# Kernel tuning notes

Measured on AMD Instinct MI355X. Metric: run time of the kernel, lower is better.

Reference implementation:

```python
import jax, jax.numpy as jnp
import numpy as np

V, E, B, C = 10000, 128, 16, 128
N_REL = 8

def setup_inputs() -> dict:
    key = jax.random.key(0)
    k1, k2, k3, k4, k5 = jax.random.split(key, 5)
    src = jax.random.randint(k1, (B, C), 0, V, dtype=jnp.int32)
    src_embed = jax.random.normal(k2, (B, C, E), dtype=jnp.float32)
    embed_weight = jax.random.normal(k3, (V, E), dtype=jnp.float32)
    edge_matrix = jax.random.uniform(k4, (V, V), dtype=jnp.float32)
    relation_matrix = jax.random.randint(k5, (V, V), 0, 9, dtype=jnp.int32)
    return {"src": src, "src_embed": src_embed, "embed_weight": embed_weight,
            "edge_matrix": edge_matrix, "relation_matrix": relation_matrix}

def reference(src, src_embed, embed_weight, edge_matrix, relation_matrix):
    # base scores against full vocab: [B, C, V]
    base = jnp.einsum('bce,ve->bcv', src_embed, embed_weight)
    # gather the rows of both tables once: [B, C, V]
    edge_rows = edge_matrix[src]
    rel_rows = relation_matrix[src]
    concept_embeddings = []
    scores = []
    for i in range(N_REL):
        # ((relation_matrix == i+1) * edge_matrix)[src] > 0, gathered form
        mask = (jnp.where(rel_rows == i + 1, edge_rows, 0.0) > 0).astype(base.dtype)
        concept_weights = mask * base                     # [B, C, V]
        attn = jax.nn.softmax(concept_weights, axis=2)     # softmax over full vocab
        ce = jnp.einsum('bcv,ve->bce', attn, embed_weight) # [B, C, E]
        concept_embeddings.append(ce)
        scores.append(jnp.sum(src_embed * ce, axis=2, keepdims=True))
    scores = jnp.concatenate(scores, axis=2)               # [B, C, 8]
    weights = jax.nn.softmax(scores, axis=2)
    final = jnp.zeros_like(src_embed)
    for i in range(N_REL):
        final = final + weights[:, :, i:i + 1] * concept_embeddings[i]
    return final
```

## Files before the change

kernel.cpp:

```cpp
#include <hip/hip_runtime.h>

#define VV 10000
#define EE 128
#define NROWS 2048
#define KS 32
#define RBSTRIDE 5120

typedef unsigned short u16;
using short8 = __attribute__((ext_vector_type(8))) short;
using f32x4  = __attribute__((ext_vector_type(4))) float;

__device__ __forceinline__ u16 f2bf(float x) {
    unsigned u = __float_as_uint(x);
    return (u16)((u + 0x7fffu + ((u >> 16) & 1u)) >> 16);
}
__device__ __forceinline__ float bf2f(u16 h) {
    return __uint_as_float(((unsigned)h) << 16);
}

__global__ __launch_bounds__(256) void k0_prep(
    const float* __restrict__ SE,
    const float* __restrict__ W,
    u16* __restrict__ SEh, u16* __restrict__ SEl,
    u16* __restrict__ Wh,  u16* __restrict__ Wl,
    u16* __restrict__ WTh, u16* __restrict__ WTl)
{
    const int u = blockIdx.x * 256 + threadIdx.x;
    float x[8];
    u16 *dh, *dl;

    if (u < 32768) {
        int fid = u >> 6, l = u & 63;
        int nf = fid >> 2, kt = fid & 3;
        int row = nf * 16 + (l & 15);
        int k0 = kt * 32 + (l >> 4) * 8;
        const float* p = SE + row * EE + k0;
        float4 a = *(const float4*)p, b = *(const float4*)(p + 4);
        x[0]=a.x; x[1]=a.y; x[2]=a.z; x[3]=a.w;
        x[4]=b.x; x[5]=b.y; x[6]=b.z; x[7]=b.w;
        dh = SEh + u * 8; dl = SEl + u * 8;
    } else if (u < 192768) {
        int u2 = u - 32768;
        int fid = u2 >> 6, l = u2 & 63;
        int vf = fid >> 2, kt = fid & 3;
        int row = vf * 16 + (l & 15);
        int k0 = kt * 32 + (l >> 4) * 8;
        const float* p = W + row * EE + k0;
        float4 a = *(const float4*)p, b = *(const float4*)(p + 4);
        x[0]=a.x; x[1]=a.y; x[2]=a.z; x[3]=a.w;
        x[4]=b.x; x[5]=b.y; x[6]=b.z; x[7]=b.w;
        dh = Wh + u2 * 8; dl = Wl + u2 * 8;
    } else {
        int u3 = u - 192768;
        int fid = u3 >> 6, l = u3 & 63;
        int ef = fid / 313, kc = fid - ef * 313;
        int e  = ef * 16 + (l & 15);
        int k8 = kc * 32 + (l >> 4) * 8;
        if (k8 < VV) {
            #pragma unroll
            for (int i = 0; i < 8; i++) x[i] = W[(k8 + i) * EE + e];
        } else {
            #pragma unroll
            for (int i = 0; i < 8; i++) x[i] = 0.f;
        }
        dh = WTh + u3 * 8; dl = WTl + u3 * 8;
    }

    short8 hv, lv;
    #pragma unroll
    for (int i = 0; i < 8; i++) {
        u16 hb = f2bf(x[i]);
        hv[i] = (short)hb;
        lv[i] = (short)f2bf(x[i] - bf2f(hb));
    }
    *(short8*)dh = hv;
    *(short8*)dl = lv;
}

__global__ __launch_bounds__(256) void k1_mfma(
    const u16* __restrict__ SEh, const u16* __restrict__ SEl,
    const u16* __restrict__ Wh,  const u16* __restrict__ Wl,
    float* __restrict__ base)
{
    const int tid = threadIdx.x;
    const int l = tid & 63, wv = tid >> 6;
    const int wn = wv >> 1, wq = wv & 1;
    const int vt = blockIdx.y, nt = blockIdx.x;
    const int nf0 = nt * 4 + wn * 2;
    const int vf0 = vt * 8 + wq * 4;

    f32x4 acc[2][4];
    #pragma unroll
    for (int i = 0; i < 2; i++)
        #pragma unroll
        for (int j = 0; j < 4; j++)
            acc[i][j] = (f32x4){0.f, 0.f, 0.f, 0.f};

    #pragma unroll
    for (int kt = 0; kt < 4; ++kt) {
        short8 ah[2], al[2];
        #pragma unroll
        for (int i = 0; i < 2; ++i) {
            int off = (((nf0 + i) * 4 + kt) * 64 + l) * 8;
            ah[i] = *(const short8*)(SEh + off);
            al[i] = *(const short8*)(SEl + off);
        }
        #pragma unroll
        for (int j = 0; j < 4; ++j) {
            int vf = vf0 + j;
            short8 bh = {0,0,0,0,0,0,0,0};
            short8 bl = {0,0,0,0,0,0,0,0};
            if (vf < 625) {
                int off = ((vf * 4 + kt) * 64 + l) * 8;
                bh = *(const short8*)(Wh + off);
                bl = *(const short8*)(Wl + off);
            }
            #pragma unroll
            for (int i = 0; i < 2; ++i) {
                acc[i][j] = __builtin_amdgcn_mfma_f32_16x16x32_bf16(ah[i], bh, acc[i][j], 0, 0, 0);
                acc[i][j] = __builtin_amdgcn_mfma_f32_16x16x32_bf16(ah[i], bl, acc[i][j], 0, 0, 0);
                acc[i][j] = __builtin_amdgcn_mfma_f32_16x16x32_bf16(al[i], bh, acc[i][j], 0, 0, 0);
            }
        }
    }

    const int c = l & 15, r0 = (l >> 4) * 4;
    #pragma unroll
    for (int j = 0; j < 4; ++j) {
        int vf = vf0 + j;
        if (vf >= 625) continue;
        int v = vf * 16 + c;
        #pragma unroll
        for (int i = 0; i < 2; ++i) {
            int n = (nf0 + i) * 16 + r0;
            #pragma unroll
            for (int r = 0; r < 4; ++r)
                base[(n + r) * VV + v] = acc[i][j][r];
        }
    }
}

__global__ __launch_bounds__(256) void k2_stats(
    const int*   __restrict__ src,
    const float* __restrict__ edge,
    const int*   __restrict__ rel,
    const float* __restrict__ baseA,
    unsigned char* __restrict__ rb4,
    float* __restrict__ cG)
{
    __shared__ float wred[33][4];
    __shared__ float fin[33];

    const int n = blockIdx.x;
    const int tid = threadIdx.x;
    const int lane = tid & 63;
    const int wv = tid >> 6;
    const int s = src[n];
    const float4* brow4 = (const float4*)(baseA + (long long)n * VV);
    const float4* erow4 = (const float4*)(edge + (long long)s * VV);
    const int4*   rrow4 = (const int4*)(rel + (long long)s * VV);
    unsigned short* crow = (unsigned short*)(rb4 + (long long)n * RBSTRIDE);

    float accv[33];
    #pragma unroll
    for (int i = 0; i < 33; i++) accv[i] = 0.f;

    for (int v4 = tid; v4 < VV / 4; v4 += 256) {
        float4 b = brow4[v4];
        float4 e = erow4[v4];
        int4   r = rrow4[v4];
        float bb[4] = {b.x, b.y, b.z, b.w};
        float ee[4] = {e.x, e.y, e.z, e.w};
        int   rr[4] = {r.x, r.y, r.z, r.w};
        unsigned pk = 0u;
        #pragma unroll
        for (int c = 0; c < 4; c++) {
            int rb = (rr[c] >= 1 && rr[c] <= 8 && ee[c] > 0.f) ? rr[c] : 0;
            float bc = bb[c];
            float eb = __expf(bc);
            float beb = bc * eb;
            pk |= ((unsigned)rb) << (4 * c);
            accv[0] += bc;
            #pragma unroll
            for (int q = 0; q < 8; q++) {
                float m = (rb == q + 1) ? 1.f : 0.f;
                accv[1 + q]  += m;
                accv[9 + q]  = fmaf(m, bc,  accv[9 + q]);
                accv[17 + q] = fmaf(m, eb,  accv[17 + q]);
                accv[25 + q] = fmaf(m, beb, accv[25 + q]);
            }
        }
        crow[v4] = (unsigned short)pk;
    }

    #pragma unroll
    for (int i = 0; i < 33; i++) {
        float x = accv[i];
        #pragma unroll
        for (int off = 32; off > 0; off >>= 1) x += __shfl_xor(x, off, 64);
        if (lane == 0) wred[i][wv] = x;
    }
    __syncthreads();
    if (tid < 33)
        fin[tid] = wred[tid][0] + wred[tid][1] + wred[tid][2] + wred[tid][3];
    __syncthreads();

    if (tid == 0) {
        float sumbase = fin[0];
        float sc[8], Z[8];
        float smax = -1e30f;
        #pragma unroll
        for (int q = 0; q < 8; q++) {
            Z[q]  = ((float)VV - fin[1 + q]) + fin[17 + q];
            sc[q] = (sumbase - fin[9 + q] + fin[25 + q]) / Z[q];
            smax = fmaxf(smax, sc[q]);
        }
        float wsum = 0.f, wq[8];
        #pragma unroll
        for (int q = 0; q < 8; q++) { wq[q] = __expf(sc[q] - smax); wsum += wq[q]; }
        float Kc = 0.f;
        float* cg = cG + n * 10;
        #pragma unroll
        for (int q = 0; q < 8; q++) {
            float c = (wq[q] / wsum) / Z[q];
            cg[1 + q] = c;
            Kc += c;
        }
        cg[0] = 0.f;
        cg[9] = Kc;
    }
}

__global__ __launch_bounds__(256) void k3_mfma(
    const float* __restrict__ baseA,
    const unsigned char* __restrict__ rb4,
    const float* __restrict__ cG,
    const u16* __restrict__ WTh, const u16* __restrict__ WTl,
    float* __restrict__ part)
{
    __shared__ float cvt[64][10];

    const int tid = threadIdx.x;
    const int l = tid & 63, wv = tid >> 6;
    const int wm = wv >> 1, we = wv & 1;
    const int mt = blockIdx.x, ks = blockIdx.y;
    const int g = l >> 4, rr_ = l & 15;
    const int kc0 = (313 * ks) / KS;
    const int kc1 = (313 * (ks + 1)) / KS;

    for (int t = tid; t < 640; t += 256)
        cvt[t / 10][t % 10] = cG[(mt * 64 + t / 10) * 10 + (t % 10)];
    __syncthreads();

    const int mf0 = mt * 4 + wm * 2;
    const int rl0 = (wm * 2) * 16 + rr_;
    const int rl1 = (wm * 2 + 1) * 16 + rr_;
    const float* arow0 = baseA + (long long)(mf0 * 16 + rr_) * VV;
    const float* arow1 = baseA + (long long)((mf0 + 1) * 16 + rr_) * VV;
    const unsigned char* rrow0 = rb4 + (long long)(mf0 * 16 + rr_) * RBSTRIDE;
    const unsigned char* rrow1 = rb4 + (long long)((mf0 + 1) * 16 + rr_) * RBSTRIDE;
    const float Kc0 = cvt[rl0][9];
    const float Kc1 = cvt[rl1][9];

    f32x4 acc[2][4];
    #pragma unroll
    for (int i = 0; i < 2; i++)
        #pragma unroll
        for (int j = 0; j < 4; j++)
            acc[i][j] = (f32x4){0.f, 0.f, 0.f, 0.f};

    for (int kc = kc0; kc < kc1; ++kc) {
        int k8 = kc * 32 + g * 8;
        short8 ah[2], al[2];

        #pragma unroll
        for (int i = 0; i < 2; ++i) {
            const float* arow = i ? arow1 : arow0;
            const unsigned char* rrow = i ? rrow1 : rrow0;
            const float Kci = i ? Kc1 : Kc0;
            const int rli = i ? rl1 : rl0;
            float x[8];
            if (k8 < VV) {
                float4 a = *(const float4*)(arow + k8);
                float4 b = *(const float4*)(arow + k8 + 4);
                unsigned cw = *(const unsigned*)(rrow + (k8 >> 1));
                float t[8] = {a.x, a.y, a.z, a.w, b.x, b.y, b.z, b.w};
                #pragma unroll
                for (int q = 0; q < 8; q++) {
                    float cc = cvt[rli][(cw >> (4 * q)) & 15u];
                    x[q] = fmaf(cc, __expf(t[q]) - 1.f, Kci);
                }
            } else {
                #pragma unroll
                for (int q = 0; q < 8; q++) x[q] = 0.f;
            }
            #pragma unroll
            for (int q = 0; q < 8; q++) {
                u16 hb = f2bf(x[q]);
                ah[i][q] = (short)hb;
                al[i][q] = (short)f2bf(x[q] - bf2f(hb));
            }
        }

        #pragma unroll
        for (int j = 0; j < 4; ++j) {
            int ef = we * 4 + j;
            int off = ((ef * 313 + kc) * 64 + l) * 8;
            short8 bh = *(const short8*)(WTh + off);
            short8 bl = *(const short8*)(WTl + off);
            #pragma unroll
            for (int i = 0; i < 2; ++i) {
                acc[i][j] = __builtin_amdgcn_mfma_f32_16x16x32_bf16(ah[i], bh, acc[i][j], 0, 0, 0);
                acc[i][j] = __builtin_amdgcn_mfma_f32_16x16x32_bf16(ah[i], bl, acc[i][j], 0, 0, 0);
                acc[i][j] = __builtin_amdgcn_mfma_f32_16x16x32_bf16(al[i], bh, acc[i][j], 0, 0, 0);
            }
        }
    }

    float* pp = part + (long long)ks * NROWS * EE;
    const int c = l & 15, r0 = g * 4;
    #pragma unroll
    for (int i = 0; i < 2; ++i) {
        #pragma unroll
        for (int j = 0; j < 4; ++j) {
            int e = (we * 4 + j) * 16 + c;
            int m = (mf0 + i) * 16 + r0;
            #pragma unroll
            for (int r = 0; r < 4; ++r)
                pp[(m + r) * EE + e] = acc[i][j][r];
        }
    }
}

__global__ __launch_bounds__(256) void k4_reduce(
    const float* __restrict__ part, float* __restrict__ out)
{
    int idx = blockIdx.x * 256 + threadIdx.x;
    const float4* p = (const float4*)part;
    const int stride = NROWS * EE / 4;
    float4 s = p[idx];
    #pragma unroll
    for (int k = 1; k < KS; k++) {
        float4 t = p[idx + k * stride];
        s.x += t.x; s.y += t.y; s.z += t.z; s.w += t.w;
    }
    ((float4*)out)[idx] = s;
}

extern "C" void kernel_launch(void* const* d_in, const int* in_sizes, int n_in,
                              void* d_out, int out_size, void* d_ws, size_t ws_size,
                              hipStream_t stream) {
    const int*   src  = (const int*)  d_in[0];
    const float* SE   = (const float*)d_in[1];
    const float* W    = (const float*)d_in[2];
    const float* edge = (const float*)d_in[3];
    const int*   rel  = (const int*)  d_in[4];
    float* out  = (float*)d_out;

    float* base = (float*)d_ws;
    float* part = base + (long long)NROWS * VV;
    u16* SEh = (u16*)(part + (long long)KS * NROWS * EE);
    u16* SEl = SEh + 262144;
    u16* Wh  = SEl + 262144;
    u16* Wl  = Wh  + 1280000;
    u16* WTh = Wl  + 1280000;
    u16* WTl = WTh + 1282048;
    unsigned char* rb4 = (unsigned char*)(WTl + 1282048);
    float* cG = (float*)(rb4 + (long long)NROWS * RBSTRIDE);

    k0_prep<<<dim3(1379), 256, 0, stream>>>(SE, W, SEh, SEl, Wh, Wl, WTh, WTl);
    k1_mfma<<<dim3(32, 79), 256, 0, stream>>>(SEh, SEl, Wh, Wl, base);
    k2_stats<<<dim3(NROWS), 256, 0, stream>>>(src, edge, rel, base, rb4, cG);
    k3_mfma<<<dim3(32, KS), 256, 0, stream>>>(base, rb4, cG, WTh, WTl, part);
    k4_reduce<<<dim3(256), 256, 0, stream>>>(part, out);
}
```

Measured before the change: 715.1 us.

## Replace split-K partial buffer and reduce kernel with atomic accumulation in k3

```diff
diff --git a/kernel.cpp b/kernel.cpp
--- a/kernel.cpp
+++ b/kernel.cpp
@@ -16,6 +16,12 @@
 }
 __device__ __forceinline__ float bf2f(u16 h) {
     return __uint_as_float(((unsigned)h) << 16);
+}
+
+__global__ __launch_bounds__(256) void kz_zero(float* __restrict__ out)
+{
+    int idx = blockIdx.x * 256 + threadIdx.x;
+    ((float4*)out)[idx] = make_float4(0.f, 0.f, 0.f, 0.f);
 }
 
 __global__ __launch_bounds__(256) void k0_prep(
@@ -236,14 +242,15 @@
     const unsigned char* __restrict__ rb4,
     const float* __restrict__ cG,
     const u16* __restrict__ WTh, const u16* __restrict__ WTl,
-    float* __restrict__ part)
+    float* __restrict__ out)
 {
     __shared__ float cvt[64][10];
 
     const int tid = threadIdx.x;
     const int l = tid & 63, wv = tid >> 6;
-    const int wm = wv >> 1, we = wv & 1;
-    const int mt = blockIdx.x, ks = blockIdx.y;
+    const int fid = blockIdx.x;
+    const int ks = (fid & 7) * 4 + (fid >> 8);
+    const int mt = (fid >> 3) & 31;
     const int g = l >> 4, rr_ = l & 15;
     const int kc0 = (313 * ks) / KS;
     const int kc1 = (313 * (ks + 1)) / KS;
@@ -252,33 +259,21 @@
         cvt[t / 10][t % 10] = cG[(mt * 64 + t / 10) * 10 + (t % 10)];
     __syncthreads();
 
-    const int mf0 = mt * 4 + wm * 2;
-    const int rl0 = (wm * 2) * 16 + rr_;
-    const int rl1 = (wm * 2 + 1) * 16 + rr_;
-    const float* arow0 = baseA + (long long)(mf0 * 16 + rr_) * VV;
-    const float* arow1 = baseA + (long long)((mf0 + 1) * 16 + rr_) * VV;
-    const unsigned char* rrow0 = rb4 + (long long)(mf0 * 16 + rr_) * RBSTRIDE;
-    const unsigned char* rrow1 = rb4 + (long long)((mf0 + 1) * 16 + rr_) * RBSTRIDE;
-    const float Kc0 = cvt[rl0][9];
-    const float Kc1 = cvt[rl1][9];
-
-    f32x4 acc[2][4];
-    #pragma unroll
-    for (int i = 0; i < 2; i++)
-        #pragma unroll
-        for (int j = 0; j < 4; j++)
-            acc[i][j] = (f32x4){0.f, 0.f, 0.f, 0.f};
+    const int mf = mt * 4 + wv;
+    const int row = mf * 16 + rr_;
+    const int rl = wv * 16 + rr_;
+    const float* arow = baseA + (long long)row * VV;
+    const unsigned char* rrow = rb4 + (long long)row * RBSTRIDE;
+    const float Kc = cvt[rl][9];
+
+    f32x4 acc[8];
+    #pragma unroll
+    for (int j = 0; j < 8; j++) acc[j] = (f32x4){0.f, 0.f, 0.f, 0.f};
 
     for (int kc = kc0; kc < kc1; ++kc) {
         int k8 = kc * 32 + g * 8;
-        short8 ah[2], al[2];
-
-        #pragma unroll
-        for (int i = 0; i < 2; ++i) {
-            const float* arow = i ? arow1 : arow0;
-            const unsigned char* rrow = i ? rrow1 : rrow0;
-            const float Kci = i ? Kc1 : Kc0;
-            const int rli = i ? rl1 : rl0;
+        short8 ah, al;
+        {
             float x[8];
             if (k8 < VV) {
                 float4 a = *(const float4*)(arow + k8);
@@ -287,8 +282,8 @@
                 float t[8] = {a.x, a.y, a.z, a.w, b.x, b.y, b.z, b.w};
                 #pragma unroll
                 for (int q = 0; q < 8; q++) {
-                    float cc = cvt[rli][(cw >> (4 * q)) & 15u];
-                    x[q] = fmaf(cc, __expf(t[q]) - 1.f, Kci);
+                    float cc = cvt[rl][(cw >> (4 * q)) & 15u];
+                    x[q] = fmaf(cc, __expf(t[q]) - 1.f, Kc);
                 }
             } else {
                 #pragma unroll
@@ -297,54 +292,31 @@
             #pragma unroll
             for (int q = 0; q < 8; q++) {
                 u16 hb = f2bf(x[q]);
-                ah[i][q] = (short)hb;
-                al[i][q] = (short)f2bf(x[q] - bf2f(hb));
-            }
-        }
-
-        #pragma unroll
-        for (int j = 0; j < 4; ++j) {
-            int ef = we * 4 + j;
-            int off = ((ef * 313 + kc) * 64 + l) * 8;
+                ah[q] = (short)hb;
+                al[q] = (short)f2bf(x[q] - bf2f(hb));
+            }
+        }
+
+        #pragma unroll
+        for (int j = 0; j < 8; ++j) {
+            int off = ((j * 313 + kc) * 64 + l) * 8;
             short8 bh = *(const short8*)(WTh + off);
             short8 bl = *(const short8*)(WTl + off);
-            #pragma unroll
-            for (int i = 0; i < 2; ++i) {
-                acc[i][j] = __builtin_amdgcn_mfma_f32_16x16x32_bf16(ah[i], bh, acc[i][j], 0, 0, 0);
-                acc[i][j] = __builtin_amdgcn_mfma_f32_16x16x32_bf16(ah[i], bl, acc[i][j], 0, 0, 0);
-                acc[i][j] = __builtin_amdgcn_mfma_f32_16x16x32_bf16(al[i], bh, acc[i][j], 0, 0, 0);
-            }
-        }
-    }
-
-    float* pp = part + (long long)ks * NROWS * EE;
+            acc[j] = __builtin_amdgcn_mfma_f32_16x16x32_bf16(ah, bh, acc[j], 0, 0, 0);
+            acc[j] = __builtin_amdgcn_mfma_f32_16x16x32_bf16(ah, bl, acc[j], 0, 0, 0);
+            acc[j] = __builtin_amdgcn_mfma_f32_16x16x32_bf16(al, bh, acc[j], 0, 0, 0);
+        }
+    }
+
     const int c = l & 15, r0 = g * 4;
     #pragma unroll
-    for (int i = 0; i < 2; ++i) {
-        #pragma unroll
-        for (int j = 0; j < 4; ++j) {
-            int e = (we * 4 + j) * 16 + c;
-            int m = (mf0 + i) * 16 + r0;
-            #pragma unroll
-            for (int r = 0; r < 4; ++r)
-                pp[(m + r) * EE + e] = acc[i][j][r];
-        }
-    }
-}
-
-__global__ __launch_bounds__(256) void k4_reduce(
-    const float* __restrict__ part, float* __restrict__ out)
-{
-    int idx = blockIdx.x * 256 + threadIdx.x;
-    const float4* p = (const float4*)part;
-    const int stride = NROWS * EE / 4;
-    float4 s = p[idx];
-    #pragma unroll
-    for (int k = 1; k < KS; k++) {
-        float4 t = p[idx + k * stride];
-        s.x += t.x; s.y += t.y; s.z += t.z; s.w += t.w;
-    }
-    ((float4*)out)[idx] = s;
+    for (int j = 0; j < 8; ++j) {
+        int e = j * 16 + c;
+        int m = mf * 16 + r0;
+        #pragma unroll
+        for (int r = 0; r < 4; ++r)
+            atomicAdd(&out[(m + r) * EE + e], acc[j][r]);
+    }
 }
 
 extern "C" void kernel_launch(void* const* d_in, const int* in_sizes, int n_in,
@@ -358,8 +330,7 @@
     float* out  = (float*)d_out;
 
     float* base = (float*)d_ws;
-    float* part = base + (long long)NROWS * VV;
-    u16* SEh = (u16*)(part + (long long)KS * NROWS * EE);
+    u16* SEh = (u16*)(base + (long long)NROWS * VV);
     u16* SEl = SEh + 262144;
     u16* Wh  = SEl + 262144;
     u16* Wl  = Wh  + 1280000;
@@ -368,9 +339,9 @@
     unsigned char* rb4 = (unsigned char*)(WTl + 1282048);
     float* cG = (float*)(rb4 + (long long)NROWS * RBSTRIDE);
 
+    kz_zero<<<dim3(256), 256, 0, stream>>>(out);
     k0_prep<<<dim3(1379), 256, 0, stream>>>(SE, W, SEh, SEl, Wh, Wl, WTh, WTl);
     k1_mfma<<<dim3(32, 79), 256, 0, stream>>>(SEh, SEl, Wh, Wl, base);
     k2_stats<<<dim3(NROWS), 256, 0, stream>>>(src, edge, rel, base, rb4, cG);
-    k3_mfma<<<dim3(32, KS), 256, 0, stream>>>(base, rb4, cG, WTh, WTl, part);
-    k4_reduce<<<dim3(256), 256, 0, stream>>>(part, out);
-}
+    k3_mfma<<<dim3(1024), 256, 0, stream>>>(base, rb4, cG, WTh, WTl, out);
+}
```

Result: slower. 736.6 us (+3.0%).
